# Performance work log

Measured on AMD Instinct MI355X. Metric: run time of the kernel, lower is better.

## Reference

```python
import jax, jax.numpy as jnp
import numpy as np

N = 50000      # nodes
E = 1600000    # edges (before self loops)
B = 512        # graphs
D = 128        # gcn dim (constant across the 3 GAT layers)
H = 1024       # hidden_dim
O = 128        # output_dim
NEG_SLOPE = 0.2


def setup_inputs() -> dict:
    key = jax.random.key(0)
    ks = jax.random.split(key, 24)
    inp = {
        "x": jax.random.normal(ks[0], (N, D), jnp.float32),
        "edge_index": jax.random.randint(ks[1], (2, E), 0, N, dtype=jnp.int64),
        "edge_weight": jax.random.uniform(ks[2], (E,), jnp.float32),
        "batch": jnp.sort(jax.random.randint(ks[3], (N,), 0, B, dtype=jnp.int64)),
    }
    s = 1.0 / np.sqrt(D)
    for i in range(3):
        k = 4 + 4 * i
        inp[f"W{i+1}"] = jax.random.normal(ks[k], (D, D), jnp.float32) * s
        inp[f"as{i+1}"] = jax.random.normal(ks[k + 1], (D,), jnp.float32) * s
        inp[f"ad{i+1}"] = jax.random.normal(ks[k + 2], (D,), jnp.float32) * s
        inp[f"b{i+1}"] = jnp.zeros((D,), jnp.float32)
    inp["Wf1"] = jax.random.normal(ks[16], (D, H), jnp.float32) * s
    inp["bf1"] = jnp.zeros((H,), jnp.float32)
    inp["Wf2"] = jax.random.normal(ks[17], (H, O), jnp.float32) * (1.0 / np.sqrt(H))
    inp["bf2"] = jnp.zeros((O,), jnp.float32)
    return inp


def gat_conv(x, src, dst, W, a_src, a_dst, b):
    """PyG GATConv, heads=1: gather -> leakyrelu -> segment softmax -> scatter-add."""
    h = x @ W                                   # [N, D]
    e = jax.nn.leaky_relu(jnp.take(h @ a_src, src) + jnp.take(h @ a_dst, dst), NEG_SLOPE)  # [E']
    m = jax.ops.segment_max(e, dst, num_segments=N)
    ex = jnp.exp(e - m[dst])
    denom = jax.ops.segment_sum(ex, dst, num_segments=N)
    alpha = ex / denom[dst]                      # segment softmax over incoming edges
    out = jax.ops.segment_sum(alpha[:, None] * h[src], dst, num_segments=N)
    return out + b


def reference(x, edge_index, edge_weight, batch,
              W1, as1, ad1, b1, W2, as2, ad2, b2, W3, as3, ad3, b3,
              Wf1, bf1, Wf2, bf2):
    # GATConv adds self loops; edge_weight is unused by GATConv (faithful to original)
    loop = jnp.arange(N, dtype=edge_index.dtype)
    src = jnp.concatenate([edge_index[0], loop])
    dst = jnp.concatenate([edge_index[1], loop])

    h = gat_conv(x, src, dst, W1, as1, ad1, b1)
    h = jax.nn.relu(gat_conv(h, src, dst, W2, as2, ad2, b2))
    h = jax.nn.relu(gat_conv(h, src, dst, W3, as3, ad3, b3))

    # global mean pool (gep)
    sums = jax.ops.segment_sum(h, batch, num_segments=B)        # [B, D]
    counts = jax.ops.segment_sum(jnp.ones((N,), h.dtype), batch, num_segments=B)
    pooled = sums / jnp.maximum(counts, 1.0)[:, None]

    # MLP head; dropout is identity at inference
    o = jax.nn.relu(pooled) @ Wf1 + bf1
    o = jax.nn.relu(o) @ Wf2 + bf2
    return o
```

## Files before the change

### kernel.cpp

```cpp
#include <hip/hip_runtime.h>
#include <cstdint>
#include <cstddef>

#define NEG_SLOPE 0.2f

typedef _Float16 f16x8 __attribute__((ext_vector_type(8)));
typedef float f32x4v __attribute__((ext_vector_type(4)));

__device__ __forceinline__ unsigned enc_f(float f) {
  unsigned u = __float_as_uint(f);
  return (u & 0x80000000u) ? ~u : (u | 0x80000000u);
}
__device__ __forceinline__ float dec_f(unsigned u) {
  return (u & 0x80000000u) ? __uint_as_float(u ^ 0x80000000u) : __uint_as_float(~u);
}

#define AST 136
#define WST 136
#define HST 132
#define SMEM_BYTES (64 * AST * 2 + 128 * WST * 2)

__global__ void k_bounds(const int* __restrict__ batch, int N, int B,
                         int* __restrict__ gstart, unsigned* __restrict__ maxPart,
                         int* __restrict__ counts) {
  int n = blockIdx.x * blockDim.x + threadIdx.x;
  if (n < 768) maxPart[n] = 0u;
  if (n >= N) return;
  counts[n] = 0;
  int cur = batch[n];
  if (n == 0) {
    for (int g = 0; g <= cur; g++) gstart[g] = 0;
  } else {
    int prev = batch[n - 1];
    for (int g = prev + 1; g <= cur; g++) gstart[g] = n;
  }
  if (n == N - 1) {
    for (int g = cur + 1; g <= B; g++) gstart[g] = N;
  }
}

__global__ void k_count_rank(const int* __restrict__ dst, int E,
                             int* counts, int* __restrict__ rank) {
  int e = blockIdx.x * blockDim.x + threadIdx.x;
  if (e < E) rank[e] = atomicAdd(&counts[dst[e]], 1);
}

__global__ __launch_bounds__(1024) void k_scan1(const int* __restrict__ counts, int N,
                                                int* __restrict__ row_ptr, int* __restrict__ part) {
  __shared__ int tmp[1024];
  int t = threadIdx.x;
  int i = blockIdx.x * 1024 + t;
  int v = (i < N) ? 1 + counts[i] : 0;
  tmp[t] = v;
  __syncthreads();
  for (int off = 1; off < 1024; off <<= 1) {
    int u = (t >= off) ? tmp[t - off] : 0;
    __syncthreads();
    tmp[t] += u;
    __syncthreads();
  }
  if (i < N) row_ptr[i + 1] = tmp[t];
  if (t == 1023) part[blockIdx.x] = tmp[t];
}

__global__ __launch_bounds__(1024) void k_scan3(int* __restrict__ row_ptr,
                                                const int* __restrict__ part, int N) {
  __shared__ int s_off;
  int bi = blockIdx.x;
  if (threadIdx.x == 0) {
    int run = 0;
    for (int b = 0; b < bi; b++) run += part[b];
    s_off = run;
    if (bi == 0) row_ptr[0] = 0;
  }
  __syncthreads();
  int i = bi * 1024 + threadIdx.x;
  if (i < N) row_ptr[i + 1] += s_off;
}

__device__ __forceinline__ void gemm_body(char* smem, float* redmax, int bx,
                                          const float* __restrict__ A32,
                                          const unsigned short* __restrict__ A16,
                                          const float* __restrict__ W,
                                          unsigned short* __restrict__ hb,
                                          const float* __restrict__ asrc,
                                          const float* __restrict__ adst,
                                          float* __restrict__ sv, float* __restrict__ dv,
                                          unsigned* __restrict__ maxSlot, int M) {
  _Float16* Ah = (_Float16*)smem;
  _Float16* Wt = (_Float16*)(smem + 64 * AST * 2);
  float*    hS = (float*)(smem + 64 * AST * 2);
  int t = threadIdx.x;
  int rowbase = bx * 64;

  if (A16) {
    for (int i = t; i < 64 * 16; i += 256) {
      int r = i >> 4, c8 = (i & 15) << 3;
      int gr = rowbase + r;
      uint4 v = make_uint4(0u, 0u, 0u, 0u);
      if (gr < M) v = *(const uint4*)&A16[(size_t)gr * 128 + c8];
      *(uint4*)&Ah[r * AST + c8] = v;
    }
  } else {
    for (int i = t; i < 64 * 32; i += 256) {
      int r = i >> 5, c4 = (i & 31) << 2;
      int gr = rowbase + r;
      float4 v = make_float4(0.f, 0.f, 0.f, 0.f);
      if (gr < M) v = *(const float4*)&A32[(size_t)gr * 128 + c4];
      _Float16 tmp[4] = {(_Float16)v.x, (_Float16)v.y, (_Float16)v.z, (_Float16)v.w};
      *(short4*)&Ah[r * AST + c4] = *(short4*)tmp;
    }
  }
  for (int i = t; i < 128 * 32; i += 256) {
    int r = i >> 5, c4 = (i & 31) << 2;
    float4 v = *(const float4*)&W[(size_t)r * 128 + c4];
    Wt[(c4 + 0) * WST + r] = (_Float16)v.x;
    Wt[(c4 + 1) * WST + r] = (_Float16)v.y;
    Wt[(c4 + 2) * WST + r] = (_Float16)v.z;
    Wt[(c4 + 3) * WST + r] = (_Float16)v.w;
  }
  __syncthreads();

  int wave = t >> 6, lane = t & 63, quad = lane >> 4, l15 = lane & 15;
  f32x4v acc[4][2];
#pragma unroll
  for (int mt = 0; mt < 4; mt++)
#pragma unroll
    for (int nt = 0; nt < 2; nt++) {
      acc[mt][nt][0] = 0.f; acc[mt][nt][1] = 0.f; acc[mt][nt][2] = 0.f; acc[mt][nt][3] = 0.f;
    }

#pragma unroll
  for (int s = 0; s < 4; s++) {
    int k0 = (s << 5) + (quad << 3);
    f16x8 af[4], bf[2];
#pragma unroll
    for (int mt = 0; mt < 4; mt++)
      af[mt] = *(f16x8*)&Ah[(mt * 16 + l15) * AST + k0];
#pragma unroll
    for (int nt = 0; nt < 2; nt++)
      bf[nt] = *(f16x8*)&Wt[(wave * 32 + nt * 16 + l15) * WST + k0];
#pragma unroll
    for (int mt = 0; mt < 4; mt++)
#pragma unroll
      for (int nt = 0; nt < 2; nt++)
        acc[mt][nt] = __builtin_amdgcn_mfma_f32_16x16x32_f16(af[mt], bf[nt], acc[mt][nt], 0, 0, 0);
  }
  __syncthreads();

#pragma unroll
  for (int mt = 0; mt < 4; mt++)
#pragma unroll
    for (int nt = 0; nt < 2; nt++)
#pragma unroll
      for (int rr = 0; rr < 4; rr++)
        hS[(mt * 16 + quad * 4 + rr) * HST + wave * 32 + nt * 16 + l15] = acc[mt][nt][rr];
  __syncthreads();

  int tx = t & 31, ty = t >> 5;
  float4 av  = *(const float4*)&asrc[tx * 4];
  float4 adv = *(const float4*)&adst[tx * 4];
  float wmax = -1e30f;
#pragma unroll
  for (int r8 = 0; r8 < 8; r8++) {
    int row = r8 * 8 + ty;
    int gr = rowbase + row;
    float4 hv = *(float4*)&hS[row * HST + tx * 4];
    float ps = hv.x * av.x + hv.y * av.y + hv.z * av.z + hv.w * av.w;
    float pd = hv.x * adv.x + hv.y * adv.y + hv.z * adv.z + hv.w * adv.w;
#pragma unroll
    for (int mask = 16; mask; mask >>= 1) {
      ps += __shfl_xor(ps, mask);
      pd += __shfl_xor(pd, mask);
    }
    if (gr < M) {
      _Float16 hq[4] = {(_Float16)hv.x, (_Float16)hv.y, (_Float16)hv.z, (_Float16)hv.w};
      *(uint2*)&hb[(size_t)gr * 128 + tx * 4] = *(uint2*)hq;
      if (tx == 0) { sv[gr] = ps; dv[gr] = pd; wmax = fmaxf(wmax, ps); }
    }
  }
#pragma unroll
  for (int mask = 32; mask; mask >>= 1) wmax = fmaxf(wmax, __shfl_xor(wmax, mask));
  if ((t & 63) == 0) redmax[t >> 6] = wmax;
  __syncthreads();
  if (t == 0) {
    float mx = fmaxf(fmaxf(redmax[0], redmax[1]), fmaxf(redmax[2], redmax[3]));
    atomicMax(&maxSlot[bx & 255], enc_f(mx));
  }
}

__global__ __launch_bounds__(256) void k_fill_gemm(const int* __restrict__ src,
                                                   const int* __restrict__ dst,
                                                   const int* __restrict__ rank, int E, int N,
                                                   const int* __restrict__ row_ptr,
                                                   int* __restrict__ col,
                                                   const float* __restrict__ A32,
                                                   const float* __restrict__ W,
                                                   unsigned short* __restrict__ hb,
                                                   const float* __restrict__ asrc,
                                                   const float* __restrict__ adst,
                                                   float* __restrict__ sv, float* __restrict__ dv,
                                                   unsigned* __restrict__ maxSlot, int Gg) {
  __shared__ __align__(16) char smem[SMEM_BYTES];
  __shared__ float redmax[4];
  int b = (int)blockIdx.x;
  bool isGemm = ((b % 9) == 4) && ((b / 9) < Gg);
  if (isGemm) {
    gemm_body(smem, redmax, b / 9, A32, (const unsigned short*)nullptr, W,
              hb, asrc, adst, sv, dv, maxSlot, N);
  } else {
    int nGemmBefore = (b >= 4) ? min((b - 4) / 9 + 1, Gg) : 0;
    int i = (b - nGemmBefore) * 256 + threadIdx.x;
    if (i < N) col[row_ptr[i]] = i;
    int e = i - N;
    if (e >= 0 && e < E) col[row_ptr[dst[e]] + 1 + rank[e]] = src[e];
  }
}

__global__ __launch_bounds__(256) void k_gemm_fused(const unsigned short* __restrict__ A16,
                                                    const float* __restrict__ W,
                                                    unsigned short* __restrict__ hb,
                                                    const float* __restrict__ asrc,
                                                    const float* __restrict__ adst,
                                                    float* __restrict__ sv, float* __restrict__ dv,
                                                    unsigned* __restrict__ maxSlot, int M) {
  __shared__ __align__(16) char smem[SMEM_BYTES];
  __shared__ float redmax[4];
  gemm_body(smem, redmax, (int)blockIdx.x, (const float*)nullptr, A16, W,
            hb, asrc, adst, sv, dv, maxSlot, M);
}

__global__ __launch_bounds__(256) void k_agg(const unsigned short* __restrict__ hb,
                                             const float* __restrict__ sv,
                                             const float* __restrict__ dv,
                                             const int* __restrict__ row_ptr,
                                             const int* __restrict__ col,
                                             const float* __restrict__ bias,
                                             const unsigned* __restrict__ maxSlot,
                                             unsigned short* __restrict__ out16,
                                             int N, int relu) {
  int wid = (int)((blockIdx.x * (size_t)blockDim.x + threadIdx.x) >> 6);
  int lane = threadIdx.x & 63;
  if (wid >= N) return;

  unsigned mp = max(max(maxSlot[lane], maxSlot[lane + 64]),
                    max(maxSlot[lane + 128], maxSlot[lane + 192]));
#pragma unroll
  for (int off = 32; off; off >>= 1) mp = max(mp, __shfl_xor(mp, off));
  float maxS = dec_f(mp);

  int beg = row_ptr[wid], end = row_ptr[wid + 1];
  float dn = dv[wid];
  float m = maxS + dn;
  m = (m > 0.f) ? m : NEG_SLOPE * m;

  int g = lane >> 4, sub = lane & 15;
  const uint32_t* hbu = (const uint32_t*)hb;
  float acc[8];
#pragma unroll
  for (int k = 0; k < 8; k++) acc[k] = 0.f;
  float dsum = 0.f;

  int j = beg + g;
  float wc = 0.f;
  uint4 hc = make_uint4(0u, 0u, 0u, 0u);
  if (j < end) {
    int sn = col[j];
    float e = sv[sn] + dn;
    e = (e > 0.f) ? e : NEG_SLOPE * e;
    wc = __expf(e - m);
    hc = *(const uint4*)(hbu + (size_t)sn * 64 + sub * 4);
  }
  j += 4;
  while (j < end) {
    int sn = col[j];
    float e = sv[sn] + dn;
    e = (e > 0.f) ? e : NEG_SLOPE * e;
    float wn = __expf(e - m);
    uint4 hn = *(const uint4*)(hbu + (size_t)sn * 64 + sub * 4);
    dsum += wc;
    const _Float16* hp = (const _Float16*)&hc;
#pragma unroll
    for (int k = 0; k < 8; k++) acc[k] += wc * (float)hp[k];
    wc = wn; hc = hn;
    j += 4;
  }
  {
    dsum += wc;
    const _Float16* hp = (const _Float16*)&hc;
#pragma unroll
    for (int k = 0; k < 8; k++) acc[k] += wc * (float)hp[k];
  }

  dsum += __shfl_xor(dsum, 16);
  dsum += __shfl_xor(dsum, 32);
#pragma unroll
  for (int k = 0; k < 8; k++) {
    acc[k] += __shfl_xor(acc[k], 16);
    acc[k] += __shfl_xor(acc[k], 32);
  }
  if (lane < 16) {
    float inv = 1.f / dsum;
    float o[8];
    const float* bp = &bias[sub * 8];
#pragma unroll
    for (int k = 0; k < 8; k++) {
      o[k] = acc[k] * inv + bp[k];
      if (relu) o[k] = fmaxf(o[k], 0.f);
    }
    _Float16 q[8];
#pragma unroll
    for (int k = 0; k < 8; k++) q[k] = (_Float16)o[k];
    *(uint4*)&out16[(size_t)wid * 128 + sub * 8] = *(uint4*)q;
  }
}

__global__ __launch_bounds__(256) void k_pool(const unsigned short* __restrict__ h16,
                                              const int* __restrict__ gstart,
                                              float* __restrict__ pooled, int B) {
  __shared__ float red[4][128];
  int b = blockIdx.x, t = threadIdx.x;
  int c = t & 63, seg = t >> 6;
  int s0 = gstart[b], s1 = gstart[b + 1];
  int cnt = s1 - s0;
  int per = (cnt + 3) >> 2;
  int n0 = s0 + seg * per;
  int n1 = min(n0 + per, s1);
  const uint32_t* hu = (const uint32_t*)h16;
  float a0 = 0.f, a1 = 0.f;
  for (int n = n0; n < n1; n++) {
    union { uint32_t u; _Float16 h[2]; } cv;
    cv.u = hu[(size_t)n * 64 + c];
    a0 += (float)cv.h[0];
    a1 += (float)cv.h[1];
  }
  if (seg) { red[seg][2 * c] = a0; red[seg][2 * c + 1] = a1; }
  __syncthreads();
  if (seg == 0) {
    a0 += red[1][2 * c] + red[2][2 * c] + red[3][2 * c];
    a1 += red[1][2 * c + 1] + red[2][2 * c + 1] + red[3][2 * c + 1];
    float inv = 1.f / (float)(cnt > 0 ? cnt : 1);
    pooled[b * 128 + 2 * c]     = fmaxf(a0 * inv, 0.f);
    pooled[b * 128 + 2 * c + 1] = fmaxf(a1 * inv, 0.f);
  }
}

__global__ __launch_bounds__(256) void k_mlp(const float* __restrict__ pooled,
                                             const float* __restrict__ Wf1,
                                             const float* __restrict__ bf1,
                                             const float* __restrict__ Wf2,
                                             const float* __restrict__ bf2,
                                             float* __restrict__ out, int B) {
  __shared__ float P[4][128];
  __shared__ float H1[4][1024];
  __shared__ float R[4][128];
  int t = threadIdx.x;
  int g0 = blockIdx.x * 4;

  for (int i = t; i < 4 * 128; i += 256) {
    int gi = i >> 7, c = i & 127;
    P[gi][c] = (g0 + gi < B) ? pooled[(size_t)(g0 + gi) * 128 + c] : 0.f;
  }
  __syncthreads();

#pragma unroll
  for (int cb = 0; cb < 4; cb++) {
    int c = cb * 256 + t;
    float a0 = 0.f, a1 = 0.f, a2 = 0.f, a3 = 0.f;
    for (int k = 0; k < 128; k++) {
      float w = Wf1[(size_t)k * 1024 + c];
      a0 += P[0][k] * w; a1 += P[1][k] * w; a2 += P[2][k] * w; a3 += P[3][k] * w;
    }
    float b = bf1[c];
    H1[0][c] = fmaxf(a0 + b, 0.f);
    H1[1][c] = fmaxf(a1 + b, 0.f);
    H1[2][c] = fmaxf(a2 + b, 0.f);
    H1[3][c] = fmaxf(a3 + b, 0.f);
  }
  __syncthreads();

  int c = t & 127, hh = t >> 7;
  float a0 = 0.f, a1 = 0.f, a2 = 0.f, a3 = 0.f;
  int k0 = hh * 512;
  for (int k = k0; k < k0 + 512; k++) {
    float w = Wf2[(size_t)k * 128 + c];
    a0 += H1[0][k] * w; a1 += H1[1][k] * w; a2 += H1[2][k] * w; a3 += H1[3][k] * w;
  }
  if (hh == 1) { R[0][c] = a0; R[1][c] = a1; R[2][c] = a2; R[3][c] = a3; }
  __syncthreads();
  if (hh == 0) {
    float b = bf2[c];
    float o0 = a0 + R[0][c] + b;
    float o1 = a1 + R[1][c] + b;
    float o2 = a2 + R[2][c] + b;
    float o3 = a3 + R[3][c] + b;
    if (g0 + 0 < B) out[(size_t)(g0 + 0) * 128 + c] = o0;
    if (g0 + 1 < B) out[(size_t)(g0 + 1) * 128 + c] = o1;
    if (g0 + 2 < B) out[(size_t)(g0 + 2) * 128 + c] = o2;
    if (g0 + 3 < B) out[(size_t)(g0 + 3) * 128 + c] = o3;
  }
}

extern "C" void kernel_launch(void* const* d_in, const int* in_sizes, int n_in,
                              void* d_out, int out_size, void* d_ws, size_t ws_size,
                              hipStream_t stream) {
  const float* x     = (const float*)d_in[0];
  const int*   ei    = (const int*)d_in[1];
  const int*   batch = (const int*)d_in[3];
  const float* W1 = (const float*)d_in[4];
  const float* as1 = (const float*)d_in[5];
  const float* ad1 = (const float*)d_in[6];
  const float* b1 = (const float*)d_in[7];
  const float* W2 = (const float*)d_in[8];
  const float* as2 = (const float*)d_in[9];
  const float* ad2 = (const float*)d_in[10];
  const float* b2 = (const float*)d_in[11];
  const float* W3 = (const float*)d_in[12];
  const float* as3 = (const float*)d_in[13];
  const float* ad3 = (const float*)d_in[14];
  const float* b3 = (const float*)d_in[15];
  const float* Wf1 = (const float*)d_in[16];
  const float* bf1 = (const float*)d_in[17];
  const float* Wf2 = (const float*)d_in[18];
  const float* bf2 = (const float*)d_in[19];

  const int N = in_sizes[0] / 128;
  const int E = in_sizes[1] / 2;
  const int B = out_size / 128;

  char* base_ws = (char*)d_ws;
  size_t off = 0;
  auto carve = [&](size_t bytes) -> void* {
    off = (off + 255) & ~(size_t)255;
    void* p = base_ws + off;
    off += bytes;
    return p;
  };
  int* counts   = (int*)carve((size_t)N * 4);
  int* row_ptr  = (int*)carve((size_t)(N + 1) * 4);
  int* rank     = (int*)carve((size_t)E * 4);
  int* col      = (int*)carve((size_t)(E + N) * 4);
  int* part     = (int*)carve(1024 * 4);
  int* gstart   = (int*)carve((size_t)(B + 1) * 4);
  unsigned* maxPart = (unsigned*)carve(768 * 4);
  float* sbuf   = (float*)carve((size_t)N * 4);
  float* dbuf   = (float*)carve((size_t)N * 4);
  unsigned short* hb  = (unsigned short*)carve((size_t)N * 128 * 2);
  unsigned short* a16 = (unsigned short*)carve((size_t)N * 128 * 2);
  float* pooled = (float*)carve((size_t)B * 128 * 4);

  const int* srcp = ei;
  const int* dstp = ei + E;
  const int nb = (N + 1023) / 1024;
  const int Gg = (N + 63) / 64;
  const int Gf = (E + N + 255) / 256;

  hipLaunchKernelGGL(k_bounds, dim3((N + 255) / 256), dim3(256), 0, stream,
                     batch, N, B, gstart, maxPart, counts);
  hipLaunchKernelGGL(k_count_rank, dim3((E + 255) / 256), dim3(256), 0, stream,
                     dstp, E, counts, rank);
  hipLaunchKernelGGL(k_scan1, dim3(nb), dim3(1024), 0, stream, counts, N, row_ptr, part);
  hipLaunchKernelGGL(k_scan3, dim3(nb), dim3(1024), 0, stream, row_ptr, part, N);

  hipLaunchKernelGGL(k_fill_gemm, dim3(Gf + Gg), dim3(256), 0, stream,
                     srcp, dstp, rank, E, N, row_ptr, col,
                     x, W1, hb, as1, ad1, sbuf, dbuf, maxPart + 0 * 256, Gg);

  hipLaunchKernelGGL(k_agg, dim3((N + 3) / 4), dim3(256), 0, stream,
                     hb, sbuf, dbuf, row_ptr, col, b1, maxPart + 0 * 256, a16, N, 0);

  hipLaunchKernelGGL(k_gemm_fused, dim3(Gg), dim3(256), 0, stream,
                     a16, W2, hb, as2, ad2, sbuf, dbuf, maxPart + 1 * 256, N);
  hipLaunchKernelGGL(k_agg, dim3((N + 3) / 4), dim3(256), 0, stream,
                     hb, sbuf, dbuf, row_ptr, col, b2, maxPart + 1 * 256, a16, N, 1);

  hipLaunchKernelGGL(k_gemm_fused, dim3(Gg), dim3(256), 0, stream,
                     a16, W3, hb, as3, ad3, sbuf, dbuf, maxPart + 2 * 256, N);
  hipLaunchKernelGGL(k_agg, dim3((N + 3) / 4), dim3(256), 0, stream,
                     hb, sbuf, dbuf, row_ptr, col, b3, maxPart + 2 * 256, a16, N, 1);

  hipLaunchKernelGGL(k_pool, dim3(B), dim3(256), 0, stream, a16, gstart, pooled, B);
  hipLaunchKernelGGL(k_mlp, dim3((B + 3) / 4), dim3(256), 0, stream,
                     pooled, Wf1, bf1, Wf2, bf2, (float*)d_out, B);
}
```

Baseline: 532.4 us.

## Use per-XCD edge counters for CSR build and double-depth prefetch in aggregation

Edge in-degree counting now uses eight per-XCD counter arrays with workgroup-scope atomics, so atomic traffic is not contended across dies. Each edge's rank is tagged with its die id. The scan kernel writes per-die base offsets and the self-loop column entries, so the fill pass only scatters real edges. The GEMM/fill block interleave stride is recomputed to match. The aggregation loop now keeps two neighbor rows in flight instead of one to hide gather latency. The cost is extra memory for the counters and reliance on the XCC id register plus a relaxed atomic scope for correctness.

```diff
diff --git a/kernel.cpp b/kernel.cpp
--- a/kernel.cpp
+++ b/kernel.cpp
@@ -3,6 +3,7 @@
 #include <cstddef>
 
 #define NEG_SLOPE 0.2f
+#define NXCD 8
 
 typedef _Float16 f16x8 __attribute__((ext_vector_type(8)));
 typedef float f32x4v __attribute__((ext_vector_type(4)));
@@ -13,6 +14,11 @@
 }
 __device__ __forceinline__ float dec_f(unsigned u) {
   return (u & 0x80000000u) ? __uint_as_float(u ^ 0x80000000u) : __uint_as_float(~u);
+}
+__device__ __forceinline__ int xcc_id() {
+  int x;
+  asm("s_getreg_b32 %0, hwreg(HW_REG_XCC_ID, 0, 4)" : "=s"(x));
+  return x & (NXCD - 1);
 }
 
 #define AST 136
@@ -22,11 +28,12 @@
 
 __global__ void k_bounds(const int* __restrict__ batch, int N, int B,
                          int* __restrict__ gstart, unsigned* __restrict__ maxPart,
-                         int* __restrict__ counts) {
+                         int* __restrict__ c) {
   int n = blockIdx.x * blockDim.x + threadIdx.x;
   if (n < 768) maxPart[n] = 0u;
   if (n >= N) return;
-  counts[n] = 0;
+#pragma unroll
+  for (int p = 0; p < NXCD; p++) c[(size_t)p * N + n] = 0;
   int cur = batch[n];
   if (n == 0) {
     for (int g = 0; g <= cur; g++) gstart[g] = 0;
@@ -39,18 +46,28 @@
   }
 }
 
-__global__ void k_count_rank(const int* __restrict__ dst, int E,
-                             int* counts, int* __restrict__ rank) {
+__global__ void k_count_rank(const int* __restrict__ dst, int E, int N,
+                             int* __restrict__ c, int* __restrict__ rank) {
+  int p = xcc_id();
   int e = blockIdx.x * blockDim.x + threadIdx.x;
-  if (e < E) rank[e] = atomicAdd(&counts[dst[e]], 1);
-}
-
-__global__ __launch_bounds__(1024) void k_scan1(const int* __restrict__ counts, int N,
+  if (e < E) {
+    int r = __hip_atomic_fetch_add(&c[(size_t)p * N + dst[e]], 1,
+                                   __ATOMIC_RELAXED, __HIP_MEMORY_SCOPE_WORKGROUP);
+    rank[e] = r | (p << 24);
+  }
+}
+
+__global__ __launch_bounds__(1024) void k_scan1(const int* __restrict__ c, int N,
                                                 int* __restrict__ row_ptr, int* __restrict__ part) {
   __shared__ int tmp[1024];
   int t = threadIdx.x;
   int i = blockIdx.x * 1024 + t;
-  int v = (i < N) ? 1 + counts[i] : 0;
+  int v = 0;
+  if (i < N) {
+    v = 1;
+#pragma unroll
+    for (int p = 0; p < NXCD; p++) v += c[(size_t)p * N + i];
+  }
   tmp[t] = v;
   __syncthreads();
   for (int off = 1; off < 1024; off <<= 1) {
@@ -64,18 +81,42 @@
 }
 
 __global__ __launch_bounds__(1024) void k_scan3(int* __restrict__ row_ptr,
-                                                const int* __restrict__ part, int N) {
+                                                const int* __restrict__ part, int N,
+                                                const int* __restrict__ c,
+                                                int* __restrict__ base, int* __restrict__ col) {
   __shared__ int s_off;
   int bi = blockIdx.x;
   if (threadIdx.x == 0) {
     int run = 0;
     for (int b = 0; b < bi; b++) run += part[b];
     s_off = run;
-    if (bi == 0) row_ptr[0] = 0;
   }
   __syncthreads();
   int i = bi * 1024 + threadIdx.x;
-  if (i < N) row_ptr[i + 1] += s_off;
+  if (i < N) {
+    int v = row_ptr[i + 1] + s_off;
+    row_ptr[i + 1] = v;
+    int node = i + 1;
+    if (node < N) {
+      col[v] = node;
+      int b = v + 1;
+#pragma unroll
+      for (int p = 0; p < NXCD; p++) {
+        base[(size_t)p * N + node] = b;
+        b += c[(size_t)p * N + node];
+      }
+    }
+    if (i == 0) {
+      row_ptr[0] = 0;
+      col[0] = 0;
+      int b = 1;
+#pragma unroll
+      for (int p = 0; p < NXCD; p++) {
+        base[(size_t)p * N] = b;
+        b += c[(size_t)p * N];
+      }
+    }
+  }
 }
 
 __device__ __forceinline__ void gemm_body(char* smem, float* redmax, int bx,
@@ -192,7 +233,7 @@
 __global__ __launch_bounds__(256) void k_fill_gemm(const int* __restrict__ src,
                                                    const int* __restrict__ dst,
                                                    const int* __restrict__ rank, int E, int N,
-                                                   const int* __restrict__ row_ptr,
+                                                   const int* __restrict__ base,
                                                    int* __restrict__ col,
                                                    const float* __restrict__ A32,
                                                    const float* __restrict__ W,
@@ -200,20 +241,24 @@
                                                    const float* __restrict__ asrc,
                                                    const float* __restrict__ adst,
                                                    float* __restrict__ sv, float* __restrict__ dv,
-                                                   unsigned* __restrict__ maxSlot, int Gg) {
+                                                   unsigned* __restrict__ maxSlot,
+                                                   int Gg, int stride) {
   __shared__ __align__(16) char smem[SMEM_BYTES];
   __shared__ float redmax[4];
   int b = (int)blockIdx.x;
-  bool isGemm = ((b % 9) == 4) && ((b / 9) < Gg);
+  bool isGemm = ((b % stride) == 0) && ((b / stride) < Gg);
   if (isGemm) {
-    gemm_body(smem, redmax, b / 9, A32, (const unsigned short*)nullptr, W,
+    gemm_body(smem, redmax, b / stride, A32, (const unsigned short*)nullptr, W,
               hb, asrc, adst, sv, dv, maxSlot, N);
   } else {
-    int nGemmBefore = (b >= 4) ? min((b - 4) / 9 + 1, Gg) : 0;
-    int i = (b - nGemmBefore) * 256 + threadIdx.x;
-    if (i < N) col[row_ptr[i]] = i;
-    int e = i - N;
-    if (e >= 0 && e < E) col[row_ptr[dst[e]] + 1 + rank[e]] = src[e];
+    int g = min(b / stride + 1, Gg);
+    int i = (b - g) * 256 + threadIdx.x;
+    if (i < E) {
+      int r = rank[i];
+      int p = r >> 24;
+      r &= 0xFFFFFF;
+      col[base[(size_t)p * N + dst[i]] + r] = src[i];
+    }
   }
 }
 
@@ -262,34 +307,49 @@
   float dsum = 0.f;
 
   int j = beg + g;
-  float wc = 0.f;
-  uint4 hc = make_uint4(0u, 0u, 0u, 0u);
+  float w0 = 0.f, w1 = 0.f;
+  uint4 h0 = make_uint4(0u, 0u, 0u, 0u), h1 = make_uint4(0u, 0u, 0u, 0u);
   if (j < end) {
     int sn = col[j];
     float e = sv[sn] + dn;
     e = (e > 0.f) ? e : NEG_SLOPE * e;
-    wc = __expf(e - m);
-    hc = *(const uint4*)(hbu + (size_t)sn * 64 + sub * 4);
-  }
-  j += 4;
+    w0 = __expf(e - m);
+    h0 = *(const uint4*)(hbu + (size_t)sn * 64 + sub * 4);
+  }
+  if (j + 4 < end) {
+    int sn = col[j + 4];
+    float e = sv[sn] + dn;
+    e = (e > 0.f) ? e : NEG_SLOPE * e;
+    w1 = __expf(e - m);
+    h1 = *(const uint4*)(hbu + (size_t)sn * 64 + sub * 4);
+  }
+  j += 8;
   while (j < end) {
+    dsum += w0;
+    {
+      const _Float16* hp = (const _Float16*)&h0;
+#pragma unroll
+      for (int k = 0; k < 8; k++) acc[k] += w0 * (float)hp[k];
+    }
+    w0 = w1; h0 = h1;
     int sn = col[j];
     float e = sv[sn] + dn;
     e = (e > 0.f) ? e : NEG_SLOPE * e;
-    float wn = __expf(e - m);
-    uint4 hn = *(const uint4*)(hbu + (size_t)sn * 64 + sub * 4);
-    dsum += wc;
-    const _Float16* hp = (const _Float16*)&hc;
-#pragma unroll
-    for (int k = 0; k < 8; k++) acc[k] += wc * (float)hp[k];
-    wc = wn; hc = hn;
+    w1 = __expf(e - m);
+    h1 = *(const uint4*)(hbu + (size_t)sn * 64 + sub * 4);
     j += 4;
   }
   {
-    dsum += wc;
-    const _Float16* hp = (const _Float16*)&hc;
-#pragma unroll
-    for (int k = 0; k < 8; k++) acc[k] += wc * (float)hp[k];
+    dsum += w0;
+    const _Float16* hp = (const _Float16*)&h0;
+#pragma unroll
+    for (int k = 0; k < 8; k++) acc[k] += w0 * (float)hp[k];
+  }
+  {
+    dsum += w1;
+    const _Float16* hp = (const _Float16*)&h1;
+#pragma unroll
+    for (int k = 0; k < 8; k++) acc[k] += w1 * (float)hp[k];
   }
 
   dsum += __shfl_xor(dsum, 16);
@@ -436,7 +496,8 @@
     off += bytes;
     return p;
   };
-  int* counts   = (int*)carve((size_t)N * 4);
+  int* c        = (int*)carve((size_t)NXCD * N * 4);
+  int* base     = (int*)carve((size_t)NXCD * N * 4);
   int* row_ptr  = (int*)carve((size_t)(N + 1) * 4);
   int* rank     = (int*)carve((size_t)E * 4);
   int* col      = (int*)carve((size_t)(E + N) * 4);
@@ -453,18 +514,19 @@
   const int* dstp = ei + E;
   const int nb = (N + 1023) / 1024;
   const int Gg = (N + 63) / 64;
-  const int Gf = (E + N + 255) / 256;
+  const int Gf = (E + 255) / 256;
+  const int stride = (Gf + Gg) / Gg;
 
   hipLaunchKernelGGL(k_bounds, dim3((N + 255) / 256), dim3(256), 0, stream,
-                     batch, N, B, gstart, maxPart, counts);
+                     batch, N, B, gstart, maxPart, c);
   hipLaunchKernelGGL(k_count_rank, dim3((E + 255) / 256), dim3(256), 0, stream,
-                     dstp, E, counts, rank);
-  hipLaunchKernelGGL(k_scan1, dim3(nb), dim3(1024), 0, stream, counts, N, row_ptr, part);
-  hipLaunchKernelGGL(k_scan3, dim3(nb), dim3(1024), 0, stream, row_ptr, part, N);
+                     dstp, E, N, c, rank);
+  hipLaunchKernelGGL(k_scan1, dim3(nb), dim3(1024), 0, stream, c, N, row_ptr, part);
+  hipLaunchKernelGGL(k_scan3, dim3(nb), dim3(1024), 0, stream, row_ptr, part, N, c, base, col);
 
   hipLaunchKernelGGL(k_fill_gemm, dim3(Gf + Gg), dim3(256), 0, stream,
-                     srcp, dstp, rank, E, N, row_ptr, col,
-                     x, W1, hb, as1, ad1, sbuf, dbuf, maxPart + 0 * 256, Gg);
+                     srcp, dstp, rank, E, N, base, col,
+                     x, W1, hb, as1, ad1, sbuf, dbuf, maxPart + 0 * 256, Gg, stride);
 
   hipLaunchKernelGGL(k_agg, dim3((N + 3) / 4), dim3(256), 0, stream,
                      hb, sbuf, dbuf, row_ptr, col, b1, maxPart + 0 * 256, a16, N, 0);
```

Result: slower. 636.7 us (+19.6%).
